# Kernel tuning notes

Hardware: AMD Instinct MI355X
Metric: run time of the kernel (lower is better)

The kernel has to match this reference:

```python
import jax, jax.numpy as jnp
import numpy as np
from jax import lax

IMG = 1280.0          # image side (80 * stride 16)
HF = WF = 80          # feature map
STRIDE = 16
A = 15                # anchors per location (5 sizes x 3 ratios)
KMIX = 5              # MDN mixture components
NIMG = 8
NGT = 32
PRE_NMS = 2000
POST_NMS = 1000
NMS_THRESH = 0.7
BATCH_PER_IMG = 256
POS_FRAC = 0.5
SCALE_CLAMP = float(np.log(1000.0 / 16.0))
LOG2PI = float(np.log(2.0 * np.pi))


def _make_anchors():
    sizes = np.array([32., 64., 128., 256., 512.])
    ratios = np.array([0.5, 1.0, 2.0])
    ws = (sizes[:, None] * np.sqrt(1.0 / ratios)[None, :]).reshape(-1)
    hs = (sizes[:, None] * np.sqrt(ratios)[None, :]).reshape(-1)
    base = np.stack([-ws / 2, -hs / 2, ws / 2, hs / 2], 1)  # [A,4]
    xs = (np.arange(WF) + 0.5) * STRIDE
    ys = (np.arange(HF) + 0.5) * STRIDE
    sx, sy = np.meshgrid(xs, ys)
    shifts = np.stack([sx.ravel(), sy.ravel(), sx.ravel(), sy.ravel()], 1)  # [HW,4]
    return jnp.asarray((shifts[:, None, :] + base[None]).reshape(-1, 4), jnp.float32)


def setup_inputs() -> dict:
    key = jax.random.key(0)
    k = jax.random.split(key, 6)
    R = HF * WF * A
    anchors = _make_anchors()                                                # [R,4]
    pi = jax.random.normal(k[0], (NIMG, KMIX, R), jnp.float32)
    mu = jax.random.normal(k[1], (NIMG, KMIX, R), jnp.float32)
    sigma = jax.random.uniform(k[2], (NIMG, KMIX, R), jnp.float32, 0.1, 1.0)
    deltas = jax.random.normal(k[3], (NIMG, R, 4), jnp.float32) * 0.1
    xy = jax.random.uniform(k[4], (NIMG, NGT, 2), jnp.float32, 0.0, 960.0)
    wh = jax.random.uniform(k[5], (NIMG, NGT, 2), jnp.float32, 20.0, 320.0)
    gt_boxes = jnp.concatenate([xy, xy + wh], -1)                            # [N,G,4]
    return {"anchors": anchors, "pi": pi, "mu": mu, "sigma": sigma,
            "deltas": deltas, "gt_boxes": gt_boxes}


def pairwise_iou(a, b):  # [M,4],[P,4] -> [M,P]
    area_a = (a[:, 2] - a[:, 0]) * (a[:, 3] - a[:, 1])
    area_b = (b[:, 2] - b[:, 0]) * (b[:, 3] - b[:, 1])
    lt = jnp.maximum(a[:, None, :2], b[None, :, :2])
    rb = jnp.minimum(a[:, None, 2:], b[None, :, 2:])
    wh = jnp.clip(rb - lt, 0.0)
    inter = wh[..., 0] * wh[..., 1]
    return inter / jnp.maximum(area_a[:, None] + area_b[None, :] - inter, 1e-9)


def apply_deltas(d, boxes):  # Box2BoxTransform.apply_deltas, weights=(1,1,1,1)
    w = boxes[:, 2] - boxes[:, 0]
    h = boxes[:, 3] - boxes[:, 1]
    cx = boxes[:, 0] + 0.5 * w
    cy = boxes[:, 1] + 0.5 * h
    dx, dy = d[:, 0], d[:, 1]
    dw = jnp.minimum(d[:, 2], SCALE_CLAMP)
    dh = jnp.minimum(d[:, 3], SCALE_CLAMP)
    pcx = dx * w + cx
    pcy = dy * h + cy
    pw = jnp.exp(dw) * w
    ph = jnp.exp(dh) * h
    return jnp.stack([pcx - 0.5 * pw, pcy - 0.5 * ph, pcx + 0.5 * pw, pcy + 0.5 * ph], 1)


def get_deltas(src, tgt):  # Box2BoxTransform.get_deltas
    sw = src[..., 2] - src[..., 0]
    sh = src[..., 3] - src[..., 1]
    scx = src[..., 0] + 0.5 * sw
    scy = src[..., 1] + 0.5 * sh
    tw = tgt[..., 2] - tgt[..., 0]
    th = tgt[..., 3] - tgt[..., 1]
    tcx = tgt[..., 0] + 0.5 * tw
    tcy = tgt[..., 1] + 0.5 * th
    return jnp.stack([(tcx - scx) / sw, (tcy - scy) / sh,
                      jnp.log(tw / sw), jnp.log(th / sh)], -1)


def _nms_image(boxes, scores, unc):  # [R,4],[R],[R,2] -> padded top proposals
    top_s, tidx = lax.top_k(scores, PRE_NMS)
    tb = jnp.clip(boxes[tidx], 0.0, IMG)   # clip to image
    tu = unc[tidx]
    iou = pairwise_iou(tb, tb)             # [PRE,PRE]
    ar = jnp.arange(PRE_NMS)

    def body(i, keep):
        sup = (iou[i] > NMS_THRESH) & (ar > i) & keep[i]
        return keep & ~sup

    keep = lax.fori_loop(0, PRE_NMS, body, jnp.ones((PRE_NMS,), bool))
    wv = tb[:, 2] - tb[:, 0]
    hv = tb[:, 3] - tb[:, 1]
    keep = keep & (wv > 0.0) & (hv > 0.0)  # min_box_size = 0
    ms = jnp.where(keep, top_s, -jnp.inf)
    out_s, oidx = lax.top_k(ms, POST_NMS)
    return tb[oidx], out_s, tu[oidx]


def _losses(anchors, pi, mu, sigma, deltas, gt_boxes):
    # label_and_sample_anchors (no_grad in torch)
    iou = lax.stop_gradient(jax.vmap(lambda g: pairwise_iou(g, anchors))(gt_boxes))  # [N,G,R]
    vals = iou.max(axis=1)                       # matched IoU quality  [N,R]
    idx = jnp.argmax(iou, axis=1)                # matched gt index     [N,R]
    labels = jnp.where(vals >= 0.7, 1, jnp.where(vals >= 0.3, -1, 0))
    best_gt = iou.max(axis=2)                    # [N,G]
    lq = jnp.any((iou >= best_gt[:, :, None] - 1e-7) & (best_gt[:, :, None] > 0), axis=1)
    labels = jnp.where(lq, 1, labels)            # allow_low_quality_matches
    # deterministic subsample to batch_size_per_image with positive_fraction
    pos = labels == 1
    neg = labels == 0
    n_pos = jnp.minimum(pos.sum(1), int(BATCH_PER_IMG * POS_FRAC))
    keep_pos = pos & (jnp.cumsum(pos, 1) <= n_pos[:, None])
    keep_neg = neg & (jnp.cumsum(neg, 1) <= (BATCH_PER_IMG - n_pos)[:, None])
    labels = jnp.where(keep_pos, 1, jnp.where(keep_neg, 0, -1))
    matched_gt = lax.stop_gradient(jax.vmap(lambda g, i: g[i])(gt_boxes, idx))  # [N,R,4]
    gt_deltas = get_deltas(lax.stop_gradient(anchors)[None], matched_gt)
    pos_mask = labels == 1
    # smooth_l1 with beta=0 -> L1, summed over positives
    loss_loc = jnp.sum(jnp.abs(deltas - gt_deltas) * pos_mask[..., None])
    valid = labels != -1
    t = jnp.clip(vals, 0.0, 1.0)
    lp = jax.nn.log_softmax(pi, axis=1)
    comp = lp - 0.5 * ((t[:, None, :] - mu) / sigma) ** 2 - jnp.log(sigma) - 0.5 * LOG2PI
    nll = -jax.nn.logsumexp(comp, axis=1)        # [N,R]
    loss_cls = jnp.sum(nll * valid)
    norm = BATCH_PER_IMG * pi.shape[0]
    return jnp.stack([loss_cls / norm, loss_loc / norm])


def reference(anchors, pi, mu, sigma, deltas, gt_boxes):
    # find_logit: pi-weighted mixture mean as objectness score
    pi_sm = jax.nn.softmax(pi, axis=1)           # [N,K,R]
    logits = jnp.sum(pi_sm * mu, axis=1)         # [N,R]
    # mdn_uncertainties: epistemic / aleatoric
    epis = jnp.sum(pi_sm * (mu - logits[:, None, :]) ** 2, axis=1)
    alea = jnp.sum(pi_sm * sigma ** 2, axis=1)
    unc = jnp.stack([epis, alea], -1)            # [N,R,2]
    # _decode_proposals
    boxes = jax.vmap(lambda d: apply_deltas(d, anchors))(deltas)  # [N,R,4]
    # find_top_rpn_proposals_uncertainty (pre-NMS topk, clip, NMS, post-NMS topk)
    prop_b, prop_s, prop_u = jax.vmap(_nms_image)(boxes, logits, unc)
    losses = _losses(anchors, pi, mu, sigma, deltas, gt_boxes)    # [loss_cls, loss_loc]
    return prop_b, prop_s, prop_u, losses
```

## Files before the change

### kernel.cpp

```cpp
#include <hip/hip_runtime.h>
#include <cstdint>
#include <cstddef>

typedef unsigned long long u64;
typedef unsigned int u32;
typedef unsigned short u16;
typedef unsigned char u8;

#define R_ANCH 96000
#define NIMG   8
#define KMIX   5
#define PRE    2000
#define POST   1000
#define NGT    32
#define NCHUNK 375
#define NBLK   48
#define MROW   2048
#define GC_STRIDE 16
#define SCAP   16

#define IMG_SZ        1280.0f
#define NMS_T         0.7f
#define SCALE_CLAMP_F 4.135166556742356f
#define HALF_L2PI     0.9189385332046727f

__device__ __forceinline__ u64 make_key(float s, int r) {
  u32 u = __float_as_uint(s);
  u = (u & 0x80000000u) ? ~u : (u | 0x80000000u);
  return ((u64)u << 32) | (u64)(0xFFFFFFFFu - (u32)r);
}

__device__ __forceinline__ float dec_score(u64 key) {
  u32 o = (u32)(key >> 32);
  u32 bits = (o & 0x80000000u) ? (o ^ 0x80000000u) : ~o;
  return __uint_as_float(bits);
}

__device__ __forceinline__ float iou_pair(float a0,float a1,float a2,float a3,
                                          float b0,float b1,float b2,float b3) {
#pragma clang fp contract(off)
  float areaA = (a2-a0)*(a3-a1);
  float areaB = (b2-b0)*(b3-b1);
  float lx=fmaxf(a0,b0), ly=fmaxf(a1,b1);
  float rx=fminf(a2,b2), ry=fminf(a3,b3);
  float iw=fmaxf(rx-lx,0.0f), ih=fmaxf(ry-ly,0.0f);
  float inter=iw*ih;
  return inter / fmaxf(areaA+areaB-inter, 1e-9f);
}

__device__ __forceinline__ u64 shfl64_xor(u64 v, int m) {
  int lo = __shfl_xor((int)(u32)v, m, 64);
  int hi = __shfl_xor((int)(u32)(v>>32), m, 64);
  return ((u64)(u32)hi<<32)|(u64)(u32)lo;
}

__device__ __forceinline__ void pick2048(const u32* __restrict__ hist, int k,
                                         int* s_i, u32* s_u,
                                         int& d_out, int& k_out, u32& cnt_out) {
  int tid = threadIdx.x;
  int lane = tid & 63, w = tid >> 6;
  u32 h[8]; u32 ssum = 0;
#pragma unroll
  for (int i=0;i<8;++i){ h[i] = hist[2047 - (tid*8 + i)]; ssum += h[i]; }
  u32 incl = ssum;
  for (int off=1; off<64; off<<=1){
    u32 t = (u32)__shfl_up((int)incl, off, 64);
    if (lane >= off) incl += t;
  }
  if (lane==63) s_i[w] = (int)incl;
  __syncthreads();
  u32 base = 0;
  for (int ww=0; ww<w; ++ww) base += (u32)s_i[ww];
  u32 run = base + incl - ssum;
#pragma unroll
  for (int i=0;i<8;++i){
    u32 nr = run + h[i];
    if (run < (u32)k && nr >= (u32)k){
      s_u[0] = (u32)(2047 - (tid*8+i));
      s_u[1] = (u32)k - run;
      s_u[2] = h[i];
    }
    run = nr;
  }
  __syncthreads();
  d_out = (int)s_u[0]; k_out = (int)s_u[1]; cnt_out = s_u[2];
  __syncthreads();
}

__global__ void kZero(u32* z, int nwords) {
  for (int i = blockIdx.x*256 + threadIdx.x; i < nwords; i += gridDim.x*256)
    z[i] = 0u;
}

__global__ __launch_bounds__(256) void kA_mdn(
    const float* __restrict__ pi, const float* __restrict__ mu,
    const float* __restrict__ sigma, float* __restrict__ logits,
    float* __restrict__ epis, float* __restrict__ alea,
    u32* __restrict__ hist0,
    const float* __restrict__ anchors, const float* __restrict__ gt,
    const float* __restrict__ deltas,
    float* __restrict__ nll_o, float* __restrict__ loc_o) {
  __shared__ u32 s_h[2048];
  __shared__ float s_gt[NGT*4];
  int tid = threadIdx.x;
  int r = blockIdx.x*256 + tid;
  int img = blockIdx.y;
  for (int b=tid; b<2048; b+=256) s_h[b]=0u;
  if (tid < NGT*4) s_gt[tid] = gt[img*NGT*4 + tid];
  size_t base = (size_t)img*KMIX*R_ANCH + r;
  float p[KMIX], m[KMIX], s[KMIX];
#pragma unroll
  for (int k=0;k<KMIX;k++){
    p[k]=pi[base+(size_t)k*R_ANCH];
    m[k]=mu[base+(size_t)k*R_ANCH];
    s[k]=sigma[base+(size_t)k*R_ANCH];
  }
  float mx = p[0];
#pragma unroll
  for (int k=1;k<KMIX;k++) mx = fmaxf(mx,p[k]);
  float e[KMIX]; float sum = 0.0f;
#pragma unroll
  for (int k=0;k<KMIX;k++){ e[k]=expf(p[k]-mx); sum += e[k]; }
  float w[KMIX]; float lg = 0.0f;
#pragma unroll
  for (int k=0;k<KMIX;k++){ w[k]=e[k]/sum; lg += w[k]*m[k]; }
  float ep = 0.0f, al = 0.0f;
#pragma unroll
  for (int k=0;k<KMIX;k++){ float d=m[k]-lg; ep += w[k]*d*d; al += w[k]*s[k]*s[k]; }
  size_t o = (size_t)img*R_ANCH + r;
  logits[o]=lg; epis[o]=ep; alea[o]=al;
  __syncthreads();
  u64 key = make_key(lg, r);
  atomicAdd(&s_h[(u32)(key>>53)], 1u);
  float4 a = ((const float4*)anchors)[r];
  float aA = (a.z-a.x)*(a.w-a.y);
  float bi = -1.0f, bu = 1.0f; int idx = 0;
#pragma unroll 4
  for (int g=0; g<NGT; ++g){
    float g0=s_gt[g*4], g1=s_gt[g*4+1], g2=s_gt[g*4+2], g3=s_gt[g*4+3];
    float ga=(g2-g0)*(g3-g1);
    float lx=fmaxf(g0,a.x), ly=fmaxf(g1,a.y);
    float rx=fminf(g2,a.z), ry=fminf(g3,a.w);
    float iw=fmaxf(rx-lx,0.0f), ih=fmaxf(ry-ly,0.0f);
    float inter=iw*ih;
    float uni = fmaxf(ga + aA - inter, 1e-9f);
    if (inter*bu > bi*uni){ bi=inter; bu=uni; idx=g; }
  }
  float vbest = bi/bu;
  float lsum = logf(sum);
  float t_ = fminf(fmaxf(vbest, 0.0f), 1.0f);
  float comp[KMIX];
#pragma unroll
  for (int k=0;k<KMIX;k++){
    float z = (t_ - m[k]) / s[k];
    comp[k] = (p[k]-mx-lsum) - 0.5f*z*z - logf(s[k]) - HALF_L2PI;
  }
  float cm = comp[0];
#pragma unroll
  for (int k=1;k<KMIX;k++) cm = fmaxf(cm, comp[k]);
  float se = 0.0f;
#pragma unroll
  for (int k=0;k<KMIX;k++) se += expf(comp[k]-cm);
  float nll = -(cm + logf(se));
  const float* gb = &s_gt[idx*4];
  float sw = a.z-a.x, sh = a.w-a.y;
  float scx = a.x+0.5f*sw, scy = a.y+0.5f*sh;
  float tw = gb[2]-gb[0], th = gb[3]-gb[1];
  float tcx = gb[0]+0.5f*tw, tcy = gb[1]+0.5f*th;
  float4 d = ((const float4*)deltas)[(size_t)img*R_ANCH + r];
  float loc = fabsf(d.x-(tcx-scx)/sw) + fabsf(d.y-(tcy-scy)/sh)
            + fabsf(d.z-logf(tw/sw)) + fabsf(d.w-logf(th/sh));
  nll_o[o] = nll; loc_o[o] = loc;
  __syncthreads();
  for (int b=tid; b<2048; b+=256){ u32 v=s_h[b]; if(v) atomicAdd(&hist0[img*2048+b], v); }
}

__global__ __launch_bounds__(256) void kL1_bestgt(const float* __restrict__ anchors,
                                                  const float* __restrict__ gt,
                                                  int* __restrict__ best) {
  __shared__ float s_gt[NGT*4];
  __shared__ float s_ga[NGT];
  __shared__ int s_best[NGT];
  int tid = threadIdx.x, img = blockIdx.y;
  if (tid < NGT*4) s_gt[tid] = gt[img*NGT*4 + tid];
  if (tid < NGT){
    const float* g4 = gt + img*NGT*4 + tid*4;
    s_ga[tid] = (g4[2]-g4[0])*(g4[3]-g4[1]);
    s_best[tid] = 0;
  }
  __syncthreads();
  float4 an[8]; float aA[8];
#pragma unroll
  for (int q=0; q<8; ++q){
    int r = blockIdx.x*256 + tid + q*(NBLK*256);
    an[q] = (r < R_ANCH) ? ((const float4*)anchors)[r]
                         : make_float4(0.f,0.f,0.f,0.f);
    aA[q] = (an[q].z-an[q].x)*(an[q].w-an[q].y);
  }
  float vmax[NGT];
#pragma unroll 2
  for (int g=0; g<NGT; ++g){
    float g0=s_gt[g*4], g1=s_gt[g*4+1], g2=s_gt[g*4+2], g3=s_gt[g*4+3];
    float ga=s_ga[g];
    float bi=0.0f, bu=1.0f;
#pragma unroll
    for (int q=0; q<8; ++q){
      float lx=fmaxf(g0,an[q].x), ly=fmaxf(g1,an[q].y);
      float rx=fminf(g2,an[q].z), ry=fminf(g3,an[q].w);
      float iw=fmaxf(rx-lx,0.0f), ih=fmaxf(ry-ly,0.0f);
      float inter=iw*ih;
      float uni=fmaxf(ga+aA[q]-inter,1e-9f);
      if (inter*bu > bi*uni){ bi=inter; bu=uni; }
    }
    vmax[g] = bi/bu;
  }
  int lane = tid & 63;
#pragma unroll
  for (int g=0; g<NGT; ++g){
    float v = vmax[g];
    v = fmaxf(v, __shfl_xor(v, 1, 64));
    v = fmaxf(v, __shfl_xor(v, 2, 64));
    v = fmaxf(v, __shfl_xor(v, 4, 64));
    v = fmaxf(v, __shfl_xor(v, 8, 64));
    v = fmaxf(v, __shfl_xor(v,16, 64));
    v = fmaxf(v, __shfl_xor(v,32, 64));
    if (lane==0 && v > 0.0f) atomicMax(&s_best[g], __float_as_int(v));
  }
  __syncthreads();
  if (tid < NGT) atomicMax(&best[img*NGT + tid], s_best[tid]);
}

__global__ __launch_bounds__(256) void kP1(const float* __restrict__ logits,
                                           const u32* __restrict__ hist0,
                                           u32* __restrict__ hist1) {
  __shared__ u32 s_h[2048];
  __shared__ int s_i[8]; __shared__ u32 s_u[3];
  int img = blockIdx.y, tid = threadIdx.x;
  int d0,k0; u32 c0;
  pick2048(hist0 + img*2048, PRE, s_i, s_u, d0,k0,c0);
  if (c0 <= 2048u) return;
  for (int b=tid; b<2048; b+=256) s_h[b]=0u;
  __syncthreads();
  const float* sc = logits + (size_t)img*R_ANCH;
  for (int r = blockIdx.x*256 + tid; r < R_ANCH; r += NBLK*256){
    u64 key = make_key(sc[r], r);
    if ((int)(key>>53) == d0) atomicAdd(&s_h[(u32)(key>>42)&2047u], 1u);
  }
  __syncthreads();
  for (int b=tid; b<2048; b+=256){ u32 v=s_h[b]; if(v) atomicAdd(&hist1[img*2048+b], v); }
}

__global__ __launch_bounds__(256) void kP2(const float* __restrict__ logits,
                                           const u32* __restrict__ hist0,
                                           const u32* __restrict__ hist1,
                                           u32* __restrict__ hist2) {
  __shared__ u32 s_h[2048];
  __shared__ int s_i[8]; __shared__ u32 s_u[3];
  int img = blockIdx.y, tid = threadIdx.x;
  int d0,k0; u32 c0;
  pick2048(hist0 + img*2048, PRE, s_i, s_u, d0,k0,c0);
  if (c0 <= 2048u) return;
  int d1,k1; u32 c1;
  pick2048(hist1 + img*2048, k0, s_i, s_u, d1,k1,c1);
  if (c1 <= 2048u) return;
  u64 p1 = ((u64)d0<<11) | (u64)d1;
  for (int b=tid; b<2048; b+=256) s_h[b]=0u;
  __syncthreads();
  const float* sc = logits + (size_t)img*R_ANCH;
  for (int r = blockIdx.x*256 + tid; r < R_ANCH; r += NBLK*256){
    u64 key = make_key(sc[r], r);
    if ((key>>42) == p1) atomicAdd(&s_h[(u32)(key>>31)&2047u], 1u);
  }
  __syncthreads();
  for (int b=tid; b<2048; b+=256){ u32 v=s_h[b]; if(v) atomicAdd(&hist2[img*2048+b], v); }
}

__global__ __launch_bounds__(256) void kGather(const float* __restrict__ logits,
    const u32* __restrict__ hist0, const u32* __restrict__ hist1,
    const u32* __restrict__ hist2, u64* __restrict__ cand, u32* __restrict__ gcnt) {
  __shared__ int s_i[8]; __shared__ u32 s_u[3];
  __shared__ u64 s_cand[2048];
  __shared__ u32 s_cnt, s_base;
  int img = blockIdx.y, tid = threadIdx.x;
  if (tid==0) s_cnt = 0u;
  int d,kk; u32 c;
  pick2048(hist0 + img*2048, PRE, s_i, s_u, d,kk,c);
  u64 p = (u64)d; int L = 0;
  if (c > 2048u){
    pick2048(hist1 + img*2048, kk, s_i, s_u, d,kk,c);
    p = (p<<11)|(u64)d; L = 1;
    if (c > 2048u){
      pick2048(hist2 + img*2048, kk, s_i, s_u, d,kk,c);
      p = (p<<11)|(u64)d; L = 2;
    }
  }
  u64 T = p << (64 - 11*(L+1));
  const float* sc = logits + (size_t)img*R_ANCH;
  int lane = tid & 63;
  for (int r = blockIdx.x*256 + tid; r < R_ANCH; r += NBLK*256){
    u64 key = make_key(sc[r], r);
    bool take = (key >= T);
    u64 b = __ballot(take);
    if (b){
      u32 base = 0;
      if (lane==0) base = atomicAdd(&s_cnt, (u32)__popcll(b));
      base = (u32)__shfl((int)base, 0, 64);
      if (take){
        u32 pos = base + (u32)__popcll(b & ((1ull<<lane)-1ull));
        if (pos < 2048u) s_cand[pos] = key;
        else {
          u32 gp = atomicAdd(&gcnt[img*GC_STRIDE], 1u);
          if (gp < 4096u) cand[(size_t)img*4096 + gp] = key;
        }
      }
    }
  }
  __syncthreads();
  u32 n = s_cnt < 2048u ? s_cnt : 2048u;
  if (tid==0) s_base = atomicAdd(&gcnt[img*GC_STRIDE], n);
  __syncthreads();
  u32 gb = s_base;
  for (u32 i=tid; i<n; i+=256)
    cand[(size_t)img*4096 + gb + i] = s_cand[i];
}

__global__ __launch_bounds__(1024) void kSort(
    const u64* __restrict__ cand, const u32* __restrict__ gcnt,
    const float* __restrict__ epis, const float* __restrict__ alea,
    const float* __restrict__ deltas, const float* __restrict__ anchors,
    float* __restrict__ tb, float* __restrict__ tu, float* __restrict__ ts) {
  __shared__ u64 s_keys[4096];
  int tid = threadIdx.x, img = blockIdx.x;
  u32 cnt = gcnt[img*GC_STRIDE];
  if (cnt > 4096u) cnt = 4096u;
  const u64* cp = cand + (size_t)img*4096;
  u64 e[4];
#pragma unroll
  for (int q=0; q<4; ++q){
    int i = tid*4 + q;
    e[q] = (i < (int)cnt) ? cp[i] : 0ull;
  }
  auto cswap = [](u64& a, u64& b, bool desc){
    bool sw = desc ? (a < b) : (a > b);
    if (sw){ u64 t=a; a=b; b=t; }
  };
  for (u32 kk=2; kk<=4096; kk<<=1){
    u32 j = kk>>1;
    while (j > 0){
      if (j >= 256){
#pragma unroll
        for (int q=0;q<4;++q) s_keys[tid*4+q] = e[q];
        __syncthreads();
        while (j >= 256){
#pragma unroll
          for (int q0=0; q0<2; ++q0){
            u32 qq = (u32)tid + (u32)q0*1024u;
            u32 i = ((qq & ~(j-1u)) << 1) | (qq & (j-1u));
            u32 pi_ = i | j;
            u64 a = s_keys[i], b = s_keys[pi_];
            bool descSeg = ((i & kk) == 0u);
            bool sw = descSeg ? (a < b) : (a > b);
            if (sw){ s_keys[i]=b; s_keys[pi_]=a; }
          }
          __syncthreads();
          j >>= 1;
        }
#pragma unroll
        for (int q=0;q<4;++q) e[q] = s_keys[tid*4+q];
        continue;
      }
      if (j >= 4){
        u32 J = j >> 2;
        bool isLow = ((tid & (int)J) == 0);
        bool dir = ((tid & (int)(kk>>2)) == 0);
        bool keepMax = (isLow == dir);
#pragma unroll
        for (int q=0;q<4;++q){
          u64 o = shfl64_xor(e[q], (int)J);
          u64 mx = (e[q] > o) ? e[q] : o;
          u64 mn = (e[q] > o) ? o : e[q];
          e[q] = keepMax ? mx : mn;
        }
      } else if (j == 2){
        bool dir = ((tid & (int)(kk>>2)) == 0);
        cswap(e[0], e[2], dir); cswap(e[1], e[3], dir);
      } else {
        if (kk == 2){
          cswap(e[0], e[1], true);
          cswap(e[2], e[3], false);
        } else {
          bool dir = ((tid & (int)(kk>>2)) == 0);
          cswap(e[0], e[1], dir); cswap(e[2], e[3], dir);
        }
      }
      j >>= 1;
    }
  }
#pragma unroll
  for (int q=0; q<4; ++q){
    int p = tid*4 + q;
    if (p < PRE){
      u64 key = e[q];
      u32 idx = 0xFFFFFFFFu - (u32)(key & 0xFFFFFFFFull);
      ts[img*PRE + p] = dec_score(key);
      float4 a = ((const float4*)anchors)[idx];
      float4 d = ((const float4*)deltas)[(size_t)img*R_ANCH + idx];
      float w = a.z - a.x, h = a.w - a.y;
      float cx = a.x + 0.5f*w, cy = a.y + 0.5f*h;
      float dw = fminf(d.z, SCALE_CLAMP_F), dh = fminf(d.w, SCALE_CLAMP_F);
      float pcx = d.x*w + cx, pcy = d.y*h + cy;
      float pw = expf(dw)*w, ph = expf(dh)*h;
      float x0 = fminf(fmaxf(pcx - 0.5f*pw, 0.0f), IMG_SZ);
      float y0 = fminf(fmaxf(pcy - 0.5f*ph, 0.0f), IMG_SZ);
      float x1 = fminf(fmaxf(pcx + 0.5f*pw, 0.0f), IMG_SZ);
      float y1 = fminf(fmaxf(pcy + 0.5f*ph, 0.0f), IMG_SZ);
      ((float4*)tb)[(size_t)img*PRE + p] = make_float4(x0,y0,x1,y1);
      size_t o = (size_t)img*R_ANCH + idx;
      ((float2*)tu)[(size_t)img*PRE + p] = make_float2(epis[o], alea[o]);
    }
  }
}

__global__ __launch_bounds__(1024) void kD_mask(const float* __restrict__ tb,
                                                u64* __restrict__ maskLT,
                                                u32* __restrict__ scnt,
                                                u16* __restrict__ slist) {
  __shared__ float4 s_tile[64];
  int tid = threadIdx.x;
  int a = blockIdx.x, img = blockIdx.y;
  const float4* tbi = (const float4*)tb + (size_t)img*PRE;
  if (tid < 64){
    int i = a*64 + tid;
    s_tile[tid] = (i < PRE) ? tbi[i] : make_float4(0.f,0.f,0.f,0.f);
  }
  __syncthreads();
  u64* outp = maskLT + ((size_t)img*32 + a)*MROW;
  u32* cnts = scnt + (size_t)img*2048;
  u16* lst  = slist + (size_t)img*2048*SCAP;
  int bmax = min(64, PRE - a*64);
  for (int j = a*64 + tid; j < MROW; j += 1024){
    u64 m = 0ull;
    if (j < PRE){
      float4 B = tbi[j];
      int blim = min(bmax, j - a*64);
      for (int b = 0; b < blim; ++b){
        float4 A = s_tile[b];
        float v = iou_pair(A.x,A.y,A.z,A.w, B.x,B.y,B.z,B.w);
        m |= (u64)(v > NMS_T) << b;
      }
    }
    outp[j] = m;
    u64 mm = m;
    while (mm){
      int b = __builtin_ctzll(mm); mm &= mm - 1ull;
      u32 slot = atomicAdd(&cnts[j], 1u);
      if (slot < SCAP) lst[(size_t)j*SCAP + slot] = (u16)(a*64 + b);
    }
  }
}

__global__ __launch_bounds__(1024) void kE_nms(const u64* __restrict__ maskLT,
                                               const u32* __restrict__ scnt,
                                               const u16* __restrict__ slist,
                                               u64* __restrict__ keep) {
  __shared__ u64 s_list64[2048*SCAP/4];
  __shared__ u16 s_cnt[2048];
  __shared__ u8  kbuf[2][2048];
  __shared__ u64 s_kw[32];
  __shared__ int s_change, s_ovf;
  int img = blockIdx.x, tid = threadIdx.x;
  const u64* gl = (const u64*)(slist + (size_t)img*2048*SCAP);
  for (int i=tid; i<2048*SCAP/4; i+=1024) s_list64[i] = gl[i];
  const u32* gc = scnt + (size_t)img*2048;
  for (int i=tid; i<2048; i+=1024) s_cnt[i] = (u16)gc[i];
  if (tid==0){ s_change = 0; s_ovf = 0; }
  __syncthreads();
  bool myovf = false;
#pragma unroll
  for (int q=0; q<2; ++q){
    int j = tid + q*1024;
    if (s_cnt[j] > SCAP) myovf = true;
    kbuf[0][j] = (j < PRE) ? 1 : 0;
  }
  if (myovf) s_ovf = 1;
  __syncthreads();
  const u64* MT = maskLT + (size_t)img*32*MROW;
  int cur = 0;
  for (int iter=0; iter<2048; ++iter){
    bool ovf = (s_ovf != 0);
    if (ovf && tid < 32){
      u64 w = 0ull;
      for (int b=0; b<64; ++b) w |= (u64)(kbuf[cur][tid*64+b] & 1) << b;
      s_kw[tid] = w;
    }
    __syncthreads();
    bool changed = false;
#pragma unroll
    for (int q=0; q<2; ++q){
      int j = tid + q*1024;
      u8 old = kbuf[cur][j];
      u8 nk = (j < PRE) ? 1 : 0;
      if (nk){
        int cnt = s_cnt[j];
        if (cnt <= SCAP){
          const u16* lp = (const u16*)&s_list64[j*(SCAP/4)];
          for (int i=0; i<cnt; ++i){
            if (kbuf[cur][lp[i]]){ nk = 0; break; }
          }
        } else {
          int amax = j >> 6;
          for (int a=0; a<=amax; ++a){
            if (MT[(size_t)a*MROW + j] & s_kw[a]){ nk = 0; break; }
          }
        }
      }
      kbuf[1-cur][j] = nk;
      changed |= (nk != old);
    }
    if (changed) s_change = 1;
    __syncthreads();
    int ch = s_change;
    __syncthreads();
    if (tid==0) s_change = 0;
    if (!ch) break;
    cur ^= 1;
  }
  if (tid < 32){
    u64 w = 0ull;
    for (int b=0; b<64; ++b) w |= (u64)(kbuf[cur][tid*64+b] & 1) << b;
    keep[img*32 + tid] = w;
  }
}

__global__ __launch_bounds__(256) void kL2_label(
    const float* __restrict__ anchors, const float* __restrict__ gt,
    const int* __restrict__ best,
    signed char* __restrict__ label, int* __restrict__ cpos, int* __restrict__ cneg) {
  __shared__ float s_gt[NGT*4];
  __shared__ float s_ga[NGT];
  __shared__ float s_bg[NGT];
  __shared__ int s_w[8];
  int tid = threadIdx.x, img = blockIdx.y;
  int r = blockIdx.x*256 + tid;
  if (tid < NGT*4) s_gt[tid] = gt[img*NGT*4 + tid];
  if (tid < NGT){
    const float* g4 = gt + img*NGT*4 + tid*4;
    s_ga[tid] = (g4[2]-g4[0])*(g4[3]-g4[1]);
    s_bg[tid] = __int_as_float(best[img*NGT + tid]);
  }
  __syncthreads();
  float4 a = ((const float4*)anchors)[r];
  float aA = (a.z-a.x)*(a.w-a.y);
  float bi=-1.0f, bu=1.0f; bool lq = false;
#pragma unroll 4
  for (int g=0; g<NGT; ++g){
    float g0=s_gt[g*4], g1=s_gt[g*4+1], g2=s_gt[g*4+2], g3=s_gt[g*4+3];
    float lx=fmaxf(g0,a.x), ly=fmaxf(g1,a.y);
    float rx=fminf(g2,a.z), ry=fminf(g3,a.w);
    float iw=fmaxf(rx-lx,0.0f), ih=fmaxf(ry-ly,0.0f);
    float inter=iw*ih;
    float uni = fmaxf(s_ga[g] + aA - inter, 1e-9f);
    if (inter*bu > bi*uni){ bi=inter; bu=uni; }
    float bg = s_bg[g];
    lq = lq || ((inter >= (bg - 1e-7f)*uni) && (bg > 0.0f));
  }
  float vbest = bi/bu;
  int lab = lq ? 1 : (vbest >= 0.7f ? 1 : (vbest >= 0.3f ? -1 : 0));
  label[(size_t)img*R_ANCH + r] = (signed char)lab;
  u64 bp = __ballot(lab==1), bn = __ballot(lab==0);
  int wid = tid>>6, lane = tid&63;
  if (lane==0){ s_w[wid*2]=__popcll(bp); s_w[wid*2+1]=__popcll(bn); }
  __syncthreads();
  if (tid==0){
    cpos[img*NCHUNK + blockIdx.x] = s_w[0]+s_w[2]+s_w[4]+s_w[6];
    cneg[img*NCHUNK + blockIdx.x] = s_w[1]+s_w[3]+s_w[5]+s_w[7];
  }
}

__global__ __launch_bounds__(512) void kL3_scan(const int* __restrict__ cpos,
                                                const int* __restrict__ cneg,
                                                int* __restrict__ opos,
                                                int* __restrict__ oneg,
                                                int* __restrict__ quota) {
  __shared__ int s_p[8], s_n[8];
  int img = blockIdx.x, tid = threadIdx.x;
  int vp=0, vn=0;
  if (tid < NCHUNK){ vp = cpos[img*NCHUNK+tid]; vn = cneg[img*NCHUNK+tid]; }
  int lane = tid&63, w = tid>>6;
  int ip=vp, in_=vn;
  for (int off=1; off<64; off<<=1){
    int tp=__shfl_up(ip,off,64), tn=__shfl_up(in_,off,64);
    if (lane>=off){ ip+=tp; in_+=tn; }
  }
  if (lane==63){ s_p[w]=ip; s_n[w]=in_; }
  __syncthreads();
  int bp=0,bn=0;
  for (int ww=0; ww<w; ++ww){ bp+=s_p[ww]; bn+=s_n[ww]; }
  if (tid < NCHUNK){
    opos[img*NCHUNK+tid] = bp+ip-vp;
    oneg[img*NCHUNK+tid] = bn+in_-vn;
  }
  if (tid==0){
    int tp=0,tn=0;
    for (int ww=0; ww<8; ++ww){ tp+=s_p[ww]; tn+=s_n[ww]; }
    int np = tp<128?tp:128;
    quota[img*2]=np; quota[img*2+1]=256-np;
  }
}

__global__ __launch_bounds__(256) void kL4_accum(
    const signed char* __restrict__ label, const float* __restrict__ nll_i,
    const float* __restrict__ loc_i, const int* __restrict__ opos,
    const int* __restrict__ oneg, const int* __restrict__ quota,
    float* __restrict__ acc) {
  __shared__ int s_wp[4], s_wn[4];
  __shared__ float s_red[8];
  int tid = threadIdx.x, img = blockIdx.y;
  int r = blockIdx.x*256 + tid;
  size_t o = (size_t)img*R_ANCH + r;
  int lab = label[o];
  bool pos = (lab==1), neg = (lab==0);
  u64 bp = __ballot(pos), bn = __ballot(neg);
  int wid = tid>>6, lane = tid&63;
  if (lane==0){ s_wp[wid]=__popcll(bp); s_wn[wid]=__popcll(bn); }
  __syncthreads();
  int pre_p = opos[img*NCHUNK + blockIdx.x];
  int pre_n = oneg[img*NCHUNK + blockIdx.x];
  for (int w=0; w<wid; ++w){ pre_p += s_wp[w]; pre_n += s_wn[w]; }
  u64 lm = (1ull<<lane) - 1ull;
  pre_p += __popcll(bp & lm);
  pre_n += __popcll(bn & lm);
  int np = quota[img*2], nn = quota[img*2+1];
  bool kp = pos && (pre_p < np);
  bool kn = neg && (pre_n < nn);
  float c_cls = (kp||kn) ? nll_i[o] : 0.0f;
  float c_loc = kp ? loc_i[o] : 0.0f;
  for (int of=32; of>0; of>>=1){
    c_cls += __shfl_down(c_cls, of, 64);
    c_loc += __shfl_down(c_loc, of, 64);
  }
  if (lane==0){ s_red[wid]=c_cls; s_red[4+wid]=c_loc; }
  __syncthreads();
  if (tid==0){
    float a = s_red[0]+s_red[1]+s_red[2]+s_red[3];
    float b = s_red[4]+s_red[5]+s_red[6]+s_red[7];
    if (a != 0.0f) atomicAdd(&acc[0], a);
    if (b != 0.0f) atomicAdd(&acc[1], b);
  }
}

__global__ __launch_bounds__(256) void kF_final(
    const float* __restrict__ tb, const float* __restrict__ tu,
    const float* __restrict__ ts, const u64* __restrict__ keepw,
    const float* __restrict__ acc, float* __restrict__ out) {
  __shared__ int s_wk[4], s_wn[4];
  __shared__ int s_kc, s_runk, s_runn;
  int tid = threadIdx.x, img = blockIdx.x;
  int wid = tid>>6, lane = tid&63;
  const u64* kw = keepw + img*32;
  const float NEG_INF = __uint_as_float(0xff800000u);
  int cnt = 0;
  for (int c=0; c<8; ++c){
    int p = c*256 + tid;
    float4 b = ((const float4*)tb)[(size_t)img*PRE + p];
    bool kp = (p < PRE) && (((kw[p>>6]>>(p&63))&1ull)!=0ull) && (b.z > b.x) && (b.w > b.y);
    cnt += kp ? 1 : 0;
  }
  for (int of=32; of>0; of>>=1) cnt += __shfl_down(cnt, of, 64);
  if (lane==0) s_wk[wid] = cnt;
  __syncthreads();
  if (tid==0){ s_kc = s_wk[0]+s_wk[1]+s_wk[2]+s_wk[3]; s_runk=0; s_runn=0; }
  __syncthreads();
  int kc = s_kc;
  for (int c=0; c<8; ++c){
    int p = c*256 + tid;
    float4 b = ((const float4*)tb)[(size_t)img*PRE + p];
    bool kp = (p < PRE) && (((kw[p>>6]>>(p&63))&1ull)!=0ull) && (b.z > b.x) && (b.w > b.y);
    u64 bk = __ballot(kp), bn = __ballot(!kp);
    if (lane==0){ s_wk[wid]=__popcll(bk); s_wn[wid]=__popcll(bn); }
    __syncthreads();
    int pk = s_runk, pn = s_runn;
    for (int w=0; w<wid; ++w){ pk += s_wk[w]; pn += s_wn[w]; }
    u64 lm = (1ull<<lane) - 1ull;
    pk += __popcll(bk & lm);
    pn += __popcll(bn & lm);
    int slot = kp ? pk : (kc + pn);
    if (slot < POST && p < PRE){
      ((float4*)out)[img*POST + slot] = b;
      out[32000 + img*POST + slot] = kp ? ts[img*PRE + p] : NEG_INF;
      ((float2*)(out + 40000))[img*POST + slot] = ((const float2*)tu)[(size_t)img*PRE + p];
    }
    __syncthreads();
    if (tid==0){
      s_runk += s_wk[0]+s_wk[1]+s_wk[2]+s_wk[3];
      s_runn += s_wn[0]+s_wn[1]+s_wn[2]+s_wn[3];
    }
    __syncthreads();
  }
  if (img==0 && tid<2) out[56000+tid] = acc[tid] * (1.0f/2048.0f);
}

extern "C" void kernel_launch(void* const* d_in, const int* in_sizes, int n_in,
                              void* d_out, int out_size, void* d_ws, size_t ws_size,
                              hipStream_t stream) {
  const float* anchors = (const float*)d_in[0];
  const float* pi      = (const float*)d_in[1];
  const float* mu      = (const float*)d_in[2];
  const float* sigma   = (const float*)d_in[3];
  const float* deltas  = (const float*)d_in[4];
  const float* gt      = (const float*)d_in[5];
  float* out = (float*)d_out;

  char* ws = (char*)d_ws;
  size_t off = 0;
  auto alloc = [&](size_t bytes) -> void* {
    void* p = (void*)(ws + off);
    off += (bytes + 255) & ~(size_t)255;
    return p;
  };
  float* logits = (float*)alloc((size_t)NIMG*R_ANCH*4);
  float* epis   = (float*)alloc((size_t)NIMG*R_ANCH*4);
  float* alea   = (float*)alloc((size_t)NIMG*R_ANCH*4);
  float* nll    = (float*)alloc((size_t)NIMG*R_ANCH*4);
  float* loc    = (float*)alloc((size_t)NIMG*R_ANCH*4);
  float* tb     = (float*)alloc((size_t)NIMG*PRE*4*4);
  float* tu     = (float*)alloc((size_t)NIMG*PRE*2*4);
  float* ts     = (float*)alloc((size_t)NIMG*PRE*4);
  u64*   maskLT = (u64*)  alloc((size_t)NIMG*32*MROW*8);
  u16*   slist  = (u16*)  alloc((size_t)NIMG*2048*SCAP*2);
  u64*   keepw  = (u64*)  alloc((size_t)NIMG*32*8);
  u64*   cand   = (u64*)  alloc((size_t)NIMG*4096*8);
  int*   cpos   = (int*)  alloc((size_t)NIMG*NCHUNK*4);
  int*   cneg   = (int*)  alloc((size_t)NIMG*NCHUNK*4);
  int*   opos   = (int*)  alloc((size_t)NIMG*NCHUNK*4);
  int*   oneg   = (int*)  alloc((size_t)NIMG*NCHUNK*4);
  int*   quota  = (int*)  alloc((size_t)NIMG*2*4);
  size_t zstart = off;
  u32*   hist0  = (u32*)  alloc((size_t)NIMG*2048*4);
  u32*   hist1  = (u32*)  alloc((size_t)NIMG*2048*4);
  u32*   hist2  = (u32*)  alloc((size_t)NIMG*2048*4);
  u32*   gcnt   = (u32*)  alloc((size_t)NIMG*GC_STRIDE*4);
  int*   best   = (int*)  alloc((size_t)NIMG*NGT*4);
  u32*   scnt   = (u32*)  alloc((size_t)NIMG*2048*4);
  float* acc    = (float*)alloc(8);
  int zwords = (int)((off - zstart) / 4);
  signed char* label = (signed char*)logits;

  kZero<<<dim3(64), dim3(256), 0, stream>>>((u32*)(ws + zstart), zwords);
  kA_mdn<<<dim3(NCHUNK, NIMG), dim3(256), 0, stream>>>(pi, mu, sigma, logits, epis, alea,
                                                       hist0, anchors, gt, deltas, nll, loc);
  kL1_bestgt<<<dim3(NBLK, NIMG), dim3(256), 0, stream>>>(anchors, gt, best);
  kP1<<<dim3(NBLK, NIMG), dim3(256), 0, stream>>>(logits, hist0, hist1);
  kP2<<<dim3(NBLK, NIMG), dim3(256), 0, stream>>>(logits, hist0, hist1, hist2);
  kGather<<<dim3(NBLK, NIMG), dim3(256), 0, stream>>>(logits, hist0, hist1, hist2, cand, gcnt);
  kSort<<<dim3(NIMG), dim3(1024), 0, stream>>>(cand, gcnt, epis, alea, deltas, anchors, tb, tu, ts);
  kD_mask<<<dim3(32, NIMG), dim3(1024), 0, stream>>>(tb, maskLT, scnt, slist);
  kE_nms<<<dim3(NIMG), dim3(1024), 0, stream>>>(maskLT, scnt, slist, keepw);
  kL2_label<<<dim3(NCHUNK, NIMG), dim3(256), 0, stream>>>(anchors, gt, best, label, cpos, cneg);
  kL3_scan<<<dim3(NIMG), dim3(512), 0, stream>>>(cpos, cneg, opos, oneg, quota);
  kL4_accum<<<dim3(NCHUNK, NIMG), dim3(256), 0, stream>>>(label, nll, loc, opos, oneg, quota, acc);
  kF_final<<<dim3(NIMG), dim3(256), 0, stream>>>(tb, tu, ts, keepw, acc, out);
}
```

Before: 293.6 us.

## Replace bitonic sort of candidates with bucketed rank-by-counting

Replaces the full 4096-element bitonic sort in the per-image top-k kernel with a histogram on the top 11 key bits, a prefix scan for bucket offsets, and a per-element rank computed by comparing only against keys in the same bucket. Each candidate then writes its decoded box directly to its rank position. This removes the many barrier-separated compare-exchange passes of the sort. In exchange it adds shared-memory atomics and a serial within-bucket scan whose cost grows with bucket skew. Candidates all share a narrow score range, so many may land in a few buckets.

```diff
diff --git a/kernel.cpp b/kernel.cpp
--- a/kernel.cpp
+++ b/kernel.cpp
@@ -46,12 +46,6 @@
   float iw=fmaxf(rx-lx,0.0f), ih=fmaxf(ry-ly,0.0f);
   float inter=iw*ih;
   return inter / fmaxf(areaA+areaB-inter, 1e-9f);
-}
-
-__device__ __forceinline__ u64 shfl64_xor(u64 v, int m) {
-  int lo = __shfl_xor((int)(u32)v, m, 64);
-  int hi = __shfl_xor((int)(u32)(v>>32), m, 64);
-  return ((u64)(u32)hi<<32)|(u64)(u32)lo;
 }
 
 __device__ __forceinline__ void pick2048(const u32* __restrict__ hist, int k,
@@ -324,91 +318,69 @@
     cand[(size_t)img*4096 + gb + i] = s_cand[i];
 }
 
-__global__ __launch_bounds__(1024) void kSort(
+__global__ __launch_bounds__(1024) void kRank(
     const u64* __restrict__ cand, const u32* __restrict__ gcnt,
     const float* __restrict__ epis, const float* __restrict__ alea,
     const float* __restrict__ deltas, const float* __restrict__ anchors,
     float* __restrict__ tb, float* __restrict__ tu, float* __restrict__ ts) {
-  __shared__ u64 s_keys[4096];
+  __shared__ u64 s_key[4096];
+  __shared__ u16 s_bidx[4096];
+  __shared__ u32 s_h[2048];
+  __shared__ u32 s_off[2048];
+  __shared__ u32 s_wsum[16];
   int tid = threadIdx.x, img = blockIdx.x;
   u32 cnt = gcnt[img*GC_STRIDE];
   if (cnt > 4096u) cnt = 4096u;
   const u64* cp = cand + (size_t)img*4096;
-  u64 e[4];
-#pragma unroll
-  for (int q=0; q<4; ++q){
-    int i = tid*4 + q;
-    e[q] = (i < (int)cnt) ? cp[i] : 0ull;
-  }
-  auto cswap = [](u64& a, u64& b, bool desc){
-    bool sw = desc ? (a < b) : (a > b);
-    if (sw){ u64 t=a; a=b; b=t; }
-  };
-  for (u32 kk=2; kk<=4096; kk<<=1){
-    u32 j = kk>>1;
-    while (j > 0){
-      if (j >= 256){
-#pragma unroll
-        for (int q=0;q<4;++q) s_keys[tid*4+q] = e[q];
-        __syncthreads();
-        while (j >= 256){
-#pragma unroll
-          for (int q0=0; q0<2; ++q0){
-            u32 qq = (u32)tid + (u32)q0*1024u;
-            u32 i = ((qq & ~(j-1u)) << 1) | (qq & (j-1u));
-            u32 pi_ = i | j;
-            u64 a = s_keys[i], b = s_keys[pi_];
-            bool descSeg = ((i & kk) == 0u);
-            bool sw = descSeg ? (a < b) : (a > b);
-            if (sw){ s_keys[i]=b; s_keys[pi_]=a; }
-          }
-          __syncthreads();
-          j >>= 1;
-        }
-#pragma unroll
-        for (int q=0;q<4;++q) e[q] = s_keys[tid*4+q];
-        continue;
-      }
-      if (j >= 4){
-        u32 J = j >> 2;
-        bool isLow = ((tid & (int)J) == 0);
-        bool dir = ((tid & (int)(kk>>2)) == 0);
-        bool keepMax = (isLow == dir);
-#pragma unroll
-        for (int q=0;q<4;++q){
-          u64 o = shfl64_xor(e[q], (int)J);
-          u64 mx = (e[q] > o) ? e[q] : o;
-          u64 mn = (e[q] > o) ? o : e[q];
-          e[q] = keepMax ? mx : mn;
-        }
-      } else if (j == 2){
-        bool dir = ((tid & (int)(kk>>2)) == 0);
-        cswap(e[0], e[2], dir); cswap(e[1], e[3], dir);
-      } else {
-        if (kk == 2){
-          cswap(e[0], e[1], true);
-          cswap(e[2], e[3], false);
-        } else {
-          bool dir = ((tid & (int)(kk>>2)) == 0);
-          cswap(e[0], e[1], dir); cswap(e[2], e[3], dir);
-        }
-      }
-      j >>= 1;
-    }
-  }
-#pragma unroll
-  for (int q=0; q<4; ++q){
-    int p = tid*4 + q;
-    if (p < PRE){
-      u64 key = e[q];
-      u32 idx = 0xFFFFFFFFu - (u32)(key & 0xFFFFFFFFull);
-      ts[img*PRE + p] = dec_score(key);
+  for (int i=tid; i<4096; i+=1024) s_key[i] = (i < (int)cnt) ? cp[i] : 0ull;
+  for (int b=tid; b<2048; b+=1024) s_h[b] = 0u;
+  __syncthreads();
+  for (int i=tid; i<(int)cnt; i+=1024)
+    atomicAdd(&s_h[(u32)(s_key[i]>>53)], 1u);
+  __syncthreads();
+  {
+    int b_hi = 2047 - 2*tid, b_lo = b_hi - 1;
+    u32 h_hi = s_h[b_hi], h_lo = s_h[b_lo];
+    u32 sum = h_hi + h_lo;
+    u32 incl = sum;
+    int lane = tid & 63, wv = tid >> 6;
+    for (int off=1; off<64; off<<=1){
+      u32 t = (u32)__shfl_up((int)incl, off, 64);
+      if (lane >= off) incl += t;
+    }
+    if (lane==63) s_wsum[wv] = incl;
+    __syncthreads();
+    u32 base = 0;
+    for (int w=0; w<wv; ++w) base += s_wsum[w];
+    u32 excl = base + incl - sum;
+    s_off[b_hi] = excl;
+    s_off[b_lo] = excl + h_hi;
+  }
+  __syncthreads();
+  for (int i=tid; i<(int)cnt; i+=1024){
+    u32 d = (u32)(s_key[i]>>53);
+    u32 slot = atomicAdd(&s_off[d], 1u);
+    s_bidx[slot] = (u16)i;
+  }
+  __syncthreads();
+  for (int i=tid; i<(int)cnt; i+=1024){
+    u64 my = s_key[i];
+    u32 d = (u32)(my>>53);
+    u32 size = s_h[d];
+    u32 bs = s_off[d] - size;
+    u32 rank = bs;
+    for (u32 q=bs; q<bs+size; ++q)
+      rank += (s_key[s_bidx[q]] > my) ? 1u : 0u;
+    if (rank < PRE){
+      int p = (int)rank;
+      u32 idx = 0xFFFFFFFFu - (u32)(my & 0xFFFFFFFFull);
+      ts[img*PRE + p] = dec_score(my);
       float4 a = ((const float4*)anchors)[idx];
-      float4 d = ((const float4*)deltas)[(size_t)img*R_ANCH + idx];
+      float4 dd = ((const float4*)deltas)[(size_t)img*R_ANCH + idx];
       float w = a.z - a.x, h = a.w - a.y;
       float cx = a.x + 0.5f*w, cy = a.y + 0.5f*h;
-      float dw = fminf(d.z, SCALE_CLAMP_F), dh = fminf(d.w, SCALE_CLAMP_F);
-      float pcx = d.x*w + cx, pcy = d.y*h + cy;
+      float dw = fminf(dd.z, SCALE_CLAMP_F), dh = fminf(dd.w, SCALE_CLAMP_F);
+      float pcx = dd.x*w + cx, pcy = dd.y*h + cy;
       float pw = expf(dw)*w, ph = expf(dh)*h;
       float x0 = fminf(fmaxf(pcx - 0.5f*pw, 0.0f), IMG_SZ);
       float y0 = fminf(fmaxf(pcy - 0.5f*ph, 0.0f), IMG_SZ);
@@ -753,7 +725,7 @@
   kP1<<<dim3(NBLK, NIMG), dim3(256), 0, stream>>>(logits, hist0, hist1);
   kP2<<<dim3(NBLK, NIMG), dim3(256), 0, stream>>>(logits, hist0, hist1, hist2);
   kGather<<<dim3(NBLK, NIMG), dim3(256), 0, stream>>>(logits, hist0, hist1, hist2, cand, gcnt);
-  kSort<<<dim3(NIMG), dim3(1024), 0, stream>>>(cand, gcnt, epis, alea, deltas, anchors, tb, tu, ts);
+  kRank<<<dim3(NIMG), dim3(1024), 0, stream>>>(cand, gcnt, epis, alea, deltas, anchors, tb, tu, ts);
   kD_mask<<<dim3(32, NIMG), dim3(1024), 0, stream>>>(tb, maskLT, scnt, slist);
   kE_nms<<<dim3(NIMG), dim3(1024), 0, stream>>>(maskLT, scnt, slist, keepw);
   kL2_label<<<dim3(NCHUNK, NIMG), dim3(256), 0, stream>>>(anchors, gt, best, label, cpos, cneg);
```

New measurement: 369.6 us. 25.9% more time.
